# Kernel optimization log

Hardware: AMD Instinct MI355X
Metric: run time of the kernel (lower is better)

Reference implementation:

```python
import jax, jax.numpy as jnp
import numpy as np

N = 100000
E = 3200000
IN_DIM = 512
HID = [64, 32, 16]
OUT_DIM = 40
BN_EPS = 1e-5


def setup_inputs() -> dict:
    key = jax.random.key(0)
    ks = jax.random.split(key, 10)
    x = jax.random.normal(ks[0], (N, IN_DIM), dtype=jnp.float32)
    edge_row = jnp.sort(jax.random.randint(ks[1], (E,), 0, N, dtype=jnp.int32))
    edge_col = jax.random.randint(ks[2], (E,), 0, N, dtype=jnp.int32)
    edge_val = jax.random.uniform(ks[3], (E,), dtype=jnp.float32)

    def xavier(k, fan_in, fan_out):
        limit = np.sqrt(6.0 / (fan_in + fan_out)).astype(np.float32)
        return jax.random.uniform(k, (fan_in, fan_out), dtype=jnp.float32, minval=-limit, maxval=limit)

    W1 = xavier(ks[4], IN_DIM, HID[0])
    W2 = xavier(ks[5], HID[0], HID[1])
    W3 = xavier(ks[6], HID[1], HID[2])
    W4 = xavier(ks[7], HID[2], OUT_DIM)
    return {
        "x": x, "edge_row": edge_row, "edge_col": edge_col, "edge_val": edge_val,
        "W1": W1, "W2": W2, "W3": W3, "W4": W4,
        "g1": jnp.ones((HID[0],), jnp.float32), "b1": jnp.zeros((HID[0],), jnp.float32),
        "g2": jnp.ones((HID[1],), jnp.float32), "b2": jnp.zeros((HID[1],), jnp.float32),
        "g3": jnp.ones((HID[2],), jnp.float32), "b3": jnp.zeros((HID[2],), jnp.float32),
    }


def _gcn_layer(h, W, edge_row, edge_col, edge_val, n_nodes):
    # support = h @ W  (dense GEMM), then SpMM: out[i] = sum_{e: row[e]=i} val[e] * support[col[e]]
    support = h @ W
    msgs = edge_val[:, None] * support[edge_col]  # gather + scale
    return jax.ops.segment_sum(msgs, edge_row, num_segments=n_nodes)


def _bn_elu(h, gamma, beta):
    # BatchNorm1d in training mode: batch statistics over the node dim, biased variance
    mean = jnp.mean(h, axis=0)
    var = jnp.var(h, axis=0)
    h = (h - mean) * jax.lax.rsqrt(var + BN_EPS) * gamma + beta
    return jax.nn.elu(h)


def reference(x, edge_row, edge_col, edge_val, W1, W2, W3, W4, g1, b1, g2, b2, g3, b3):
    n = x.shape[0]
    h = _gcn_layer(x, W1, edge_row, edge_col, edge_val, n)
    h = _bn_elu(h, g1, b1)  # dropout is identity in eval mode
    h = _gcn_layer(h, W2, edge_row, edge_col, edge_val, n)
    h = _bn_elu(h, g2, b2)
    h = _gcn_layer(h, W3, edge_row, edge_col, edge_val, n)
    h = _bn_elu(h, g3, b3)
    h = _gcn_layer(h, W4, edge_row, edge_col, edge_val, n)
    return jax.nn.log_softmax(h, axis=1)
```

## Files before the change

### kernel.cpp

```cpp
#include <hip/hip_runtime.h>
#include <hip/hip_bf16.h>
#include <math.h>

typedef __attribute__((ext_vector_type(8))) short short8;
typedef __attribute__((ext_vector_type(4))) float floatx4;

__global__ void rowptr_k(const int* __restrict__ erow, int* __restrict__ rp, int n, int e) {
    int i = blockIdx.x * blockDim.x + threadIdx.x;
    if (i > n) return;
    int lo = 0, hi = e;
    while (lo < hi) {
        int mid = (lo + hi) >> 1;
        if (erow[mid] < i) lo = mid + 1; else hi = mid;
    }
    rp[i] = lo;
}

__global__ void zero_k(float* __restrict__ p) {
    int i = threadIdx.x;
    if (i < 224) p[i] = 0.f;
}

__device__ __forceinline__ float elu_f(float t) {
    return t > 0.f ? t : expm1f(t);
}

__device__ __forceinline__ unsigned short f2bf(float f) {
    unsigned int u = __float_as_uint(f);
    u = (u + 0x7FFFu + ((u >> 16) & 1u)) >> 16;
    return (unsigned short)u;
}

__device__ __forceinline__ unsigned int f2bf2(float lo, float hi) {
    unsigned int a = __float_as_uint(lo);
    unsigned int b = __float_as_uint(hi);
    a = (a + 0x7FFFu + ((a >> 16) & 1u)) >> 16;
    b = (b + 0x7FFFu + ((b >> 16) & 1u)) & 0xFFFF0000u;
    return a | b;
}

__global__ __launch_bounds__(256) void w1bf_k(const float* __restrict__ W,
                                              unsigned short* __restrict__ Wb) {
    int idx = blockIdx.x * 256 + threadIdx.x;
    int n = idx >> 9, k = idx & 511;
    Wb[idx] = f2bf(W[(long)k * 64 + n]);
}

__global__ __launch_bounds__(256) void gemm1_mfma_k(const float* __restrict__ X,
                                                    const unsigned short* __restrict__ Wb,
                                                    float* __restrict__ out, int nrows) {
    const int lane = threadIdx.x & 63;
    const int wid  = threadIdx.x >> 6;
    const int lrow = lane & 15;
    const int quad = lane >> 4;
    const int m0   = (blockIdx.x * 4 + wid) * 16;
    if (m0 >= nrows) return;

    int arow = m0 + lrow;
    if (arow >= nrows) arow = nrows - 1;
    const float* __restrict__ xrow = X + (long)arow * 512 + quad * 8;
    const unsigned short* __restrict__ brow = Wb + lrow * 512 + quad * 8;

    floatx4 acc[4];
#pragma unroll
    for (int ni = 0; ni < 4; ++ni) acc[ni] = (floatx4){0.f, 0.f, 0.f, 0.f};

    float4 ca0 = *(const float4*)(xrow + 0);
    float4 ca1 = *(const float4*)(xrow + 4);
    short8 cb[4];
#pragma unroll
    for (int ni = 0; ni < 4; ++ni) cb[ni] = *(const short8*)(brow + ni * 8192);

#pragma unroll
    for (int kc = 0; kc < 16; ++kc) {
        float4 na0, na1;
        short8 nb[4];
        if (kc < 15) {
            const float* xp = xrow + (kc + 1) * 32;
            na0 = *(const float4*)(xp + 0);
            na1 = *(const float4*)(xp + 4);
#pragma unroll
            for (int ni = 0; ni < 4; ++ni)
                nb[ni] = *(const short8*)(brow + ni * 8192 + (kc + 1) * 32);
        }
        union { short8 s; unsigned int u[4]; } af;
        af.u[0] = f2bf2(ca0.x, ca0.y);
        af.u[1] = f2bf2(ca0.z, ca0.w);
        af.u[2] = f2bf2(ca1.x, ca1.y);
        af.u[3] = f2bf2(ca1.z, ca1.w);
#pragma unroll
        for (int ni = 0; ni < 4; ++ni)
            acc[ni] = __builtin_amdgcn_mfma_f32_16x16x32_bf16(af.s, cb[ni], acc[ni], 0, 0, 0);
        if (kc < 15) {
            ca0 = na0; ca1 = na1;
#pragma unroll
            for (int ni = 0; ni < 4; ++ni) cb[ni] = nb[ni];
        }
    }

#pragma unroll
    for (int r = 0; r < 4; ++r) {
        int gr = m0 + quad * 4 + r;
        if (gr < nrows) {
#pragma unroll
            for (int ni = 0; ni < 4; ++ni)
                out[(long)gr * 64 + ni * 16 + lrow] = acc[ni][r];
        }
    }
}

template<int K, int NC, bool BN>
__global__ __launch_bounds__(256) void gemm_k(const float* __restrict__ X,
                                              const float* __restrict__ W,
                                              const float* __restrict__ stats,
                                              const float* __restrict__ gamma,
                                              const float* __restrict__ beta,
                                              float* __restrict__ out, int nrows) {
    constexpr int KT = (K < 64) ? K : 64;
    constexpr int S  = KT + 4;
    __shared__ float xs[64 * S];
    __shared__ float ws[KT * NC];
    __shared__ float sc[KT];
    __shared__ float sh[KT];

    const int tid  = threadIdx.x;
    const int c    = tid & 63;
    const int rg   = tid >> 6;
    const int row0 = blockIdx.x * 64;

    if (BN) {
        if (tid < K) {
            float s1 = stats[tid], s2 = stats[K + tid];
            float mean = s1 / (float)nrows;
            float var  = s2 / (float)nrows - mean * mean;
            float rstd = rsqrtf(var + 1e-5f);
            float scl  = gamma[tid] * rstd;
            sc[tid] = scl;
            sh[tid] = beta[tid] - mean * scl;
        }
        __syncthreads();
    }

    float acc[16];
#pragma unroll
    for (int i = 0; i < 16; ++i) acc[i] = 0.f;

    for (int k0 = 0; k0 < K; k0 += KT) {
        for (int idx = tid * 4; idx < 64 * KT; idx += 1024) {
            int r = idx / KT, k = idx - r * KT;
            int gr = row0 + r;
            float4 v = make_float4(0.f, 0.f, 0.f, 0.f);
            if (gr < nrows) v = *(const float4*)&X[(long)gr * K + k0 + k];
            if (BN) {
                v.x = elu_f(v.x * sc[k + 0] + sh[k + 0]);
                v.y = elu_f(v.y * sc[k + 1] + sh[k + 1]);
                v.z = elu_f(v.z * sc[k + 2] + sh[k + 2]);
                v.w = elu_f(v.w * sc[k + 3] + sh[k + 3]);
            }
            *(float4*)&xs[r * S + k] = v;
        }
        for (int idx = tid * 4; idx < KT * NC; idx += 1024) {
            *(float4*)&ws[idx] = *(const float4*)&W[k0 * NC + idx];
        }
        __syncthreads();

        if (c < NC) {
            for (int kk = 0; kk < KT; kk += 4) {
                float w0 = ws[(kk + 0) * NC + c];
                float w1 = ws[(kk + 1) * NC + c];
                float w2 = ws[(kk + 2) * NC + c];
                float w3 = ws[(kk + 3) * NC + c];
#pragma unroll
                for (int i = 0; i < 16; ++i) {
                    const float4 xv = *(const float4*)&xs[(rg * 16 + i) * S + kk];
                    acc[i] += xv.x * w0 + xv.y * w1 + xv.z * w2 + xv.w * w3;
                }
            }
        }
        __syncthreads();
    }

    if (c < NC) {
#pragma unroll
        for (int i = 0; i < 16; ++i) {
            int gr = row0 + rg * 16 + i;
            if (gr < nrows) out[(long)gr * NC + c] = acc[i];
        }
    }
}

template<int F>
__global__ __launch_bounds__(256) void spmm_k(const int* __restrict__ rp,
                                              const int* __restrict__ ecol,
                                              const float* __restrict__ ev,
                                              const float* __restrict__ sup,
                                              float* __restrict__ out, int n) {
    constexpr int NPW = 64 / F;
    const int lane = threadIdx.x & 63;
    const int wid  = (blockIdx.x * blockDim.x + threadIdx.x) >> 6;
    const int sub  = lane / F;
    const int c    = lane - sub * F;
    const int node = wid * NPW + sub;
    if (node >= n) return;
    int s = rp[node], e = rp[node + 1];
    if (NPW == 1) {
        s = __builtin_amdgcn_readfirstlane(s);
        e = __builtin_amdgcn_readfirstlane(e);
    }
    const float* __restrict__ supc = sup + c;
    float a0 = 0.f, a1 = 0.f, a2 = 0.f, a3 = 0.f;
    int i = s;
    for (; i + 8 <= e; i += 8) {
        int   k0 = ecol[i + 0], k1 = ecol[i + 1], k2 = ecol[i + 2], k3 = ecol[i + 3];
        int   k4 = ecol[i + 4], k5 = ecol[i + 5], k6 = ecol[i + 6], k7 = ecol[i + 7];
        float v0 = ev[i + 0], v1 = ev[i + 1], v2 = ev[i + 2], v3 = ev[i + 3];
        float v4 = ev[i + 4], v5 = ev[i + 5], v6 = ev[i + 6], v7 = ev[i + 7];
        float g0 = supc[(long)k0 * F], g1 = supc[(long)k1 * F];
        float g2 = supc[(long)k2 * F], g3 = supc[(long)k3 * F];
        float g4 = supc[(long)k4 * F], g5 = supc[(long)k5 * F];
        float g6 = supc[(long)k6 * F], g7 = supc[(long)k7 * F];
        a0 += v0 * g0; a1 += v1 * g1; a2 += v2 * g2; a3 += v3 * g3;
        a0 += v4 * g4; a1 += v5 * g5; a2 += v6 * g6; a3 += v7 * g7;
    }
    for (; i < e; ++i) a0 += ev[i] * supc[(long)ecol[i] * F];
    out[(long)node * F + c] = (a0 + a1) + (a2 + a3);
}

__global__ __launch_bounds__(256) void spmm4_k(const int* __restrict__ rp,
                                               const int* __restrict__ ecol,
                                               const float* __restrict__ ev,
                                               const float* __restrict__ sup,
                                               float* __restrict__ out, int n) {
    const int lane = threadIdx.x & 63;
    const int node = (blockIdx.x * blockDim.x + threadIdx.x) >> 6;
    const bool valid = (lane < 40) && (node < n);
    float acc = -INFINITY;
    if (node < n) {
        int s = rp[node], e = rp[node + 1];
        s = __builtin_amdgcn_readfirstlane(s);
        e = __builtin_amdgcn_readfirstlane(e);
        if (lane < 40) {
            const float* __restrict__ supc = sup + lane;
            float a0 = 0.f, a1 = 0.f, a2 = 0.f, a3 = 0.f;
            int i = s;
            for (; i + 8 <= e; i += 8) {
                int   k0 = ecol[i + 0], k1 = ecol[i + 1], k2 = ecol[i + 2], k3 = ecol[i + 3];
                int   k4 = ecol[i + 4], k5 = ecol[i + 5], k6 = ecol[i + 6], k7 = ecol[i + 7];
                float v0 = ev[i + 0], v1 = ev[i + 1], v2 = ev[i + 2], v3 = ev[i + 3];
                float v4 = ev[i + 4], v5 = ev[i + 5], v6 = ev[i + 6], v7 = ev[i + 7];
                float g0 = supc[(long)k0 * 40], g1 = supc[(long)k1 * 40];
                float g2 = supc[(long)k2 * 40], g3 = supc[(long)k3 * 40];
                float g4 = supc[(long)k4 * 40], g5 = supc[(long)k5 * 40];
                float g6 = supc[(long)k6 * 40], g7 = supc[(long)k7 * 40];
                a0 += v0 * g0; a1 += v1 * g1; a2 += v2 * g2; a3 += v3 * g3;
                a0 += v4 * g4; a1 += v5 * g5; a2 += v6 * g6; a3 += v7 * g7;
            }
            for (; i < e; ++i) a0 += ev[i] * supc[(long)ecol[i] * 40];
            acc = (a0 + a1) + (a2 + a3);
        }
    }
    float m = acc;
#pragma unroll
    for (int o = 32; o; o >>= 1) m = fmaxf(m, __shfl_xor(m, o, 64));
    float p = valid ? expf(acc - m) : 0.f;
    float ssum = p;
#pragma unroll
    for (int o = 32; o; o >>= 1) ssum += __shfl_xor(ssum, o, 64);
    if (valid) out[(long)node * 40 + lane] = acc - m - logf(ssum);
}

template<int F>
__global__ __launch_bounds__(256) void stats_k(const float* __restrict__ h,
                                               float* __restrict__ stats, int n) {
    __shared__ float sm1[256];
    __shared__ float sm2[256];
    const int tid = threadIdx.x;
    float s1 = 0.f, s2 = 0.f;
    const long total = (long)n * F;
    for (long idx = (long)blockIdx.x * 256 + tid; idx < total; idx += (long)gridDim.x * 256) {
        float v = h[idx];
        s1 += v;
        s2 += v * v;
    }
    sm1[tid] = s1;
    sm2[tid] = s2;
    __syncthreads();
    if (tid < F) {
#pragma unroll
        for (int j = 1; j < 256 / F; ++j) {
            s1 += sm1[tid + j * F];
            s2 += sm2[tid + j * F];
        }
        atomicAdd(&stats[tid], s1);
        atomicAdd(&stats[F + tid], s2);
    }
}

extern "C" void kernel_launch(void* const* d_in, const int* in_sizes, int n_in,
                              void* d_out, int out_size, void* d_ws, size_t ws_size,
                              hipStream_t stream) {
    const float* x    = (const float*)d_in[0];
    const int*   erow = (const int*)d_in[1];
    const int*   ecol = (const int*)d_in[2];
    const float* ev   = (const float*)d_in[3];
    const float* W1   = (const float*)d_in[4];
    const float* W2   = (const float*)d_in[5];
    const float* W3   = (const float*)d_in[6];
    const float* W4   = (const float*)d_in[7];
    const float* g1   = (const float*)d_in[8];
    const float* b1   = (const float*)d_in[9];
    const float* g2   = (const float*)d_in[10];
    const float* b2   = (const float*)d_in[11];
    const float* g3   = (const float*)d_in[12];
    const float* b3   = (const float*)d_in[13];

    const int N = in_sizes[0] / 512;
    const int E = in_sizes[1];

    char* w = (char*)d_ws;
    int* rp = (int*)w;
    size_t off = (((size_t)(N + 1) * 4) + 255) & ~(size_t)255;
    float* stats = (float*)(w + off);
    float* A = stats + 256;
    float* B = A + (size_t)N * 64;
    unsigned short* Wb = (unsigned short*)(B + (size_t)N * 64);
    float* outp = (float*)d_out;

    const int gblocks = (N + 63) / 64;

    rowptr_k<<<(N + 1 + 255) / 256, 256, 0, stream>>>(erow, rp, N, E);
    zero_k<<<1, 256, 0, stream>>>(stats);
    w1bf_k<<<128, 256, 0, stream>>>(W1, Wb);

    {
        int mfrags = (N + 15) / 16;
        gemm1_mfma_k<<<(mfrags + 3) / 4, 256, 0, stream>>>(x, Wb, A, N);
    }
    spmm_k<64><<<(N + 3) / 4, 256, 0, stream>>>(rp, ecol, ev, A, B, N);
    stats_k<64><<<512, 256, 0, stream>>>(B, stats, N);

    gemm_k<64, 32, true><<<gblocks, 256, 0, stream>>>(B, W2, stats, g1, b1, A, N);
    {
        int waves = (N + 1) / 2;
        spmm_k<32><<<(waves + 3) / 4, 256, 0, stream>>>(rp, ecol, ev, A, B, N);
    }
    stats_k<32><<<512, 256, 0, stream>>>(B, stats + 128, N);

    gemm_k<32, 16, true><<<gblocks, 256, 0, stream>>>(B, W3, stats + 128, g2, b2, A, N);
    {
        int waves = (N + 3) / 4;
        spmm_k<16><<<(waves + 3) / 4, 256, 0, stream>>>(rp, ecol, ev, A, B, N);
    }
    stats_k<16><<<512, 256, 0, stream>>>(B, stats + 192, N);

    gemm_k<16, 40, true><<<gblocks, 256, 0, stream>>>(B, W4, stats + 192, g3, b3, A, N);
    spmm4_k<<<(N + 3) / 4, 256, 0, stream>>>(rp, ecol, ev, A, outp, N);
}
```

Before: 789.5 us.

## Store intermediates in bf16, use MFMA for small GEMMs, edge-parallel SpMM

Intermediate feature matrices are now stored as bf16 instead of fp32, which halves gather and stream traffic in the SpMM, stats and GEMM kernels. The small hidden-layer GEMMs move from scalar FMA in shared memory to bf16 MFMA, with BN+ELU fused into the A-operand load. The SpMM kernels now assign one wavefront per node and spread that node's edges across lane groups, each lane loading a vector of bf16 features, then reduce across lanes with shuffles. The cost is bf16 rounding of activations and of the small weights, which lowers accuracy.

```diff
diff --git a/kernel.cpp b/kernel.cpp
--- a/kernel.cpp
+++ b/kernel.cpp
@@ -39,6 +39,9 @@
     return a | b;
 }
 
+__device__ __forceinline__ float bflo(unsigned int d) { return __uint_as_float(d << 16); }
+__device__ __forceinline__ float bfhi(unsigned int d) { return __uint_as_float(d & 0xFFFF0000u); }
+
 __global__ __launch_bounds__(256) void w1bf_k(const float* __restrict__ W,
                                               unsigned short* __restrict__ Wb) {
     int idx = blockIdx.x * 256 + threadIdx.x;
@@ -46,9 +49,30 @@
     Wb[idx] = f2bf(W[(long)k * 64 + n]);
 }
 
+__global__ __launch_bounds__(256) void wsmall_k(const float* __restrict__ W2,
+                                                const float* __restrict__ W3,
+                                                const float* __restrict__ W4,
+                                                unsigned short* __restrict__ Wb2,
+                                                unsigned short* __restrict__ Wb3,
+                                                unsigned short* __restrict__ Wb4) {
+    int idx = blockIdx.x * 256 + threadIdx.x;
+    if (idx < 2048) {
+        int n = idx >> 6, k = idx & 63;
+        Wb2[idx] = f2bf(W2[(long)k * 32 + n]);
+    }
+    if (idx < 512) {
+        int n = idx >> 5, k = idx & 31;
+        Wb3[idx] = f2bf(W3[(long)k * 16 + n]);
+    }
+    if (idx < 1536) {
+        int n = idx >> 5, k = idx & 31;
+        Wb4[idx] = (n < 40 && k < 16) ? f2bf(W4[(long)k * 40 + n]) : (unsigned short)0;
+    }
+}
+
 __global__ __launch_bounds__(256) void gemm1_mfma_k(const float* __restrict__ X,
                                                     const unsigned short* __restrict__ Wb,
-                                                    float* __restrict__ out, int nrows) {
+                                                    unsigned short* __restrict__ out, int nrows) {
     const int lane = threadIdx.x & 63;
     const int wid  = threadIdx.x >> 6;
     const int lrow = lane & 15;
@@ -104,195 +128,211 @@
         if (gr < nrows) {
 #pragma unroll
             for (int ni = 0; ni < 4; ++ni)
-                out[(long)gr * 64 + ni * 16 + lrow] = acc[ni][r];
-        }
-    }
-}
-
-template<int K, int NC, bool BN>
-__global__ __launch_bounds__(256) void gemm_k(const float* __restrict__ X,
-                                              const float* __restrict__ W,
-                                              const float* __restrict__ stats,
-                                              const float* __restrict__ gamma,
-                                              const float* __restrict__ beta,
-                                              float* __restrict__ out, int nrows) {
-    constexpr int KT = (K < 64) ? K : 64;
-    constexpr int S  = KT + 4;
-    __shared__ float xs[64 * S];
-    __shared__ float ws[KT * NC];
-    __shared__ float sc[KT];
-    __shared__ float sh[KT];
-
-    const int tid  = threadIdx.x;
-    const int c    = tid & 63;
-    const int rg   = tid >> 6;
-    const int row0 = blockIdx.x * 64;
-
-    if (BN) {
-        if (tid < K) {
-            float s1 = stats[tid], s2 = stats[K + tid];
-            float mean = s1 / (float)nrows;
-            float var  = s2 / (float)nrows - mean * mean;
-            float rstd = rsqrtf(var + 1e-5f);
-            float scl  = gamma[tid] * rstd;
-            sc[tid] = scl;
-            sh[tid] = beta[tid] - mean * scl;
-        }
-        __syncthreads();
-    }
-
-    float acc[16];
-#pragma unroll
-    for (int i = 0; i < 16; ++i) acc[i] = 0.f;
-
-    for (int k0 = 0; k0 < K; k0 += KT) {
-        for (int idx = tid * 4; idx < 64 * KT; idx += 1024) {
-            int r = idx / KT, k = idx - r * KT;
-            int gr = row0 + r;
-            float4 v = make_float4(0.f, 0.f, 0.f, 0.f);
-            if (gr < nrows) v = *(const float4*)&X[(long)gr * K + k0 + k];
-            if (BN) {
-                v.x = elu_f(v.x * sc[k + 0] + sh[k + 0]);
-                v.y = elu_f(v.y * sc[k + 1] + sh[k + 1]);
-                v.z = elu_f(v.z * sc[k + 2] + sh[k + 2]);
-                v.w = elu_f(v.w * sc[k + 3] + sh[k + 3]);
-            }
-            *(float4*)&xs[r * S + k] = v;
-        }
-        for (int idx = tid * 4; idx < KT * NC; idx += 1024) {
-            *(float4*)&ws[idx] = *(const float4*)&W[k0 * NC + idx];
-        }
-        __syncthreads();
-
-        if (c < NC) {
-            for (int kk = 0; kk < KT; kk += 4) {
-                float w0 = ws[(kk + 0) * NC + c];
-                float w1 = ws[(kk + 1) * NC + c];
-                float w2 = ws[(kk + 2) * NC + c];
-                float w3 = ws[(kk + 3) * NC + c];
-#pragma unroll
-                for (int i = 0; i < 16; ++i) {
-                    const float4 xv = *(const float4*)&xs[(rg * 16 + i) * S + kk];
-                    acc[i] += xv.x * w0 + xv.y * w1 + xv.z * w2 + xv.w * w3;
-                }
-            }
-        }
-        __syncthreads();
-    }
-
-    if (c < NC) {
-#pragma unroll
-        for (int i = 0; i < 16; ++i) {
-            int gr = row0 + rg * 16 + i;
-            if (gr < nrows) out[(long)gr * NC + c] = acc[i];
+                out[(long)gr * 64 + ni * 16 + lrow] = f2bf(acc[ni][r]);
+        }
+    }
+}
+
+template<int K, int KP, int NF, int NSTR>
+__global__ __launch_bounds__(256) void gemmS_k(const unsigned short* __restrict__ H,
+                                               const unsigned short* __restrict__ Wb,
+                                               const float* __restrict__ stats,
+                                               const float* __restrict__ gamma,
+                                               const float* __restrict__ beta,
+                                               unsigned short* __restrict__ out,
+                                               int nrows) {
+    __shared__ __align__(16) float scs[K];
+    __shared__ __align__(16) float shs[K];
+    const int tid = threadIdx.x;
+    if (tid < K) {
+        float s1 = stats[tid], s2 = stats[K + tid];
+        float mean = s1 / (float)nrows;
+        float var  = s2 / (float)nrows - mean * mean;
+        float rstd = rsqrtf(var + 1e-5f);
+        float scl  = gamma[tid] * rstd;
+        scs[tid] = scl;
+        shs[tid] = beta[tid] - mean * scl;
+    }
+    __syncthreads();
+
+    const int lane = tid & 63;
+    const int wid  = tid >> 6;
+    const int lrow = lane & 15;
+    const int quad = lane >> 4;
+    const int m0   = (blockIdx.x * 4 + wid) * 16;
+    if (m0 >= nrows) return;
+
+    int arow = m0 + lrow;
+    if (arow >= nrows) arow = nrows - 1;
+    const unsigned short* __restrict__ hrow = H + (long)arow * K;
+
+    floatx4 acc[NF];
+#pragma unroll
+    for (int ni = 0; ni < NF; ++ni) acc[ni] = (floatx4){0.f, 0.f, 0.f, 0.f};
+
+#pragma unroll
+    for (int kc = 0; kc < KP; kc += 32) {
+        const int k8 = kc + quad * 8;
+        union { short8 s; unsigned int u[4]; } af;
+        if (k8 < K) {
+            uint4 d = *(const uint4*)(hrow + k8);
+            float4 sc0 = *(const float4*)&scs[k8];
+            float4 sc1 = *(const float4*)&scs[k8 + 4];
+            float4 sh0 = *(const float4*)&shs[k8];
+            float4 sh1 = *(const float4*)&shs[k8 + 4];
+            float f0 = elu_f(bflo(d.x) * sc0.x + sh0.x);
+            float f1 = elu_f(bfhi(d.x) * sc0.y + sh0.y);
+            float f2 = elu_f(bflo(d.y) * sc0.z + sh0.z);
+            float f3 = elu_f(bfhi(d.y) * sc0.w + sh0.w);
+            float f4 = elu_f(bflo(d.z) * sc1.x + sh1.x);
+            float f5 = elu_f(bfhi(d.z) * sc1.y + sh1.y);
+            float f6 = elu_f(bflo(d.w) * sc1.z + sh1.z);
+            float f7 = elu_f(bfhi(d.w) * sc1.w + sh1.w);
+            af.u[0] = f2bf2(f0, f1);
+            af.u[1] = f2bf2(f2, f3);
+            af.u[2] = f2bf2(f4, f5);
+            af.u[3] = f2bf2(f6, f7);
+        } else {
+            af.u[0] = af.u[1] = af.u[2] = af.u[3] = 0u;
+        }
+#pragma unroll
+        for (int ni = 0; ni < NF; ++ni) {
+            short8 bf = *(const short8*)&Wb[(ni * 16 + lrow) * KP + k8];
+            acc[ni] = __builtin_amdgcn_mfma_f32_16x16x32_bf16(af.s, bf, acc[ni], 0, 0, 0);
+        }
+    }
+
+#pragma unroll
+    for (int r = 0; r < 4; ++r) {
+        int gr = m0 + quad * 4 + r;
+        if (gr < nrows) {
+#pragma unroll
+            for (int ni = 0; ni < NF; ++ni)
+                out[(long)gr * NSTR + ni * 16 + lrow] = f2bf(acc[ni][r]);
         }
     }
 }
 
 template<int F>
-__global__ __launch_bounds__(256) void spmm_k(const int* __restrict__ rp,
-                                              const int* __restrict__ ecol,
-                                              const float* __restrict__ ev,
-                                              const float* __restrict__ sup,
-                                              float* __restrict__ out, int n) {
-    constexpr int NPW = 64 / F;
-    const int lane = threadIdx.x & 63;
-    const int wid  = (blockIdx.x * blockDim.x + threadIdx.x) >> 6;
-    const int sub  = lane / F;
-    const int c    = lane - sub * F;
-    const int node = wid * NPW + sub;
-    if (node >= n) return;
-    int s = rp[node], e = rp[node + 1];
-    if (NPW == 1) {
-        s = __builtin_amdgcn_readfirstlane(s);
-        e = __builtin_amdgcn_readfirstlane(e);
-    }
-    const float* __restrict__ supc = sup + c;
-    float a0 = 0.f, a1 = 0.f, a2 = 0.f, a3 = 0.f;
-    int i = s;
-    for (; i + 8 <= e; i += 8) {
-        int   k0 = ecol[i + 0], k1 = ecol[i + 1], k2 = ecol[i + 2], k3 = ecol[i + 3];
-        int   k4 = ecol[i + 4], k5 = ecol[i + 5], k6 = ecol[i + 6], k7 = ecol[i + 7];
-        float v0 = ev[i + 0], v1 = ev[i + 1], v2 = ev[i + 2], v3 = ev[i + 3];
-        float v4 = ev[i + 4], v5 = ev[i + 5], v6 = ev[i + 6], v7 = ev[i + 7];
-        float g0 = supc[(long)k0 * F], g1 = supc[(long)k1 * F];
-        float g2 = supc[(long)k2 * F], g3 = supc[(long)k3 * F];
-        float g4 = supc[(long)k4 * F], g5 = supc[(long)k5 * F];
-        float g6 = supc[(long)k6 * F], g7 = supc[(long)k7 * F];
-        a0 += v0 * g0; a1 += v1 * g1; a2 += v2 * g2; a3 += v3 * g3;
-        a0 += v4 * g4; a1 += v5 * g5; a2 += v6 * g6; a3 += v7 * g7;
-    }
-    for (; i < e; ++i) a0 += ev[i] * supc[(long)ecol[i] * F];
-    out[(long)node * F + c] = (a0 + a1) + (a2 + a3);
-}
-
-__global__ __launch_bounds__(256) void spmm4_k(const int* __restrict__ rp,
+__global__ __launch_bounds__(256) void spmmb_k(const int* __restrict__ rp,
                                                const int* __restrict__ ecol,
                                                const float* __restrict__ ev,
-                                               const float* __restrict__ sup,
-                                               float* __restrict__ out, int n) {
+                                               const unsigned short* __restrict__ sup,
+                                               unsigned short* __restrict__ out, int n) {
+    constexpr int GL = F / 4;
+    constexpr int G  = 64 / GL;
     const int lane = threadIdx.x & 63;
     const int node = (blockIdx.x * blockDim.x + threadIdx.x) >> 6;
-    const bool valid = (lane < 40) && (node < n);
-    float acc = -INFINITY;
-    if (node < n) {
-        int s = rp[node], e = rp[node + 1];
-        s = __builtin_amdgcn_readfirstlane(s);
-        e = __builtin_amdgcn_readfirstlane(e);
-        if (lane < 40) {
-            const float* __restrict__ supc = sup + lane;
-            float a0 = 0.f, a1 = 0.f, a2 = 0.f, a3 = 0.f;
-            int i = s;
-            for (; i + 8 <= e; i += 8) {
-                int   k0 = ecol[i + 0], k1 = ecol[i + 1], k2 = ecol[i + 2], k3 = ecol[i + 3];
-                int   k4 = ecol[i + 4], k5 = ecol[i + 5], k6 = ecol[i + 6], k7 = ecol[i + 7];
-                float v0 = ev[i + 0], v1 = ev[i + 1], v2 = ev[i + 2], v3 = ev[i + 3];
-                float v4 = ev[i + 4], v5 = ev[i + 5], v6 = ev[i + 6], v7 = ev[i + 7];
-                float g0 = supc[(long)k0 * 40], g1 = supc[(long)k1 * 40];
-                float g2 = supc[(long)k2 * 40], g3 = supc[(long)k3 * 40];
-                float g4 = supc[(long)k4 * 40], g5 = supc[(long)k5 * 40];
-                float g6 = supc[(long)k6 * 40], g7 = supc[(long)k7 * 40];
-                a0 += v0 * g0; a1 += v1 * g1; a2 += v2 * g2; a3 += v3 * g3;
-                a0 += v4 * g4; a1 += v5 * g5; a2 += v6 * g6; a3 += v7 * g7;
-            }
-            for (; i < e; ++i) a0 += ev[i] * supc[(long)ecol[i] * 40];
-            acc = (a0 + a1) + (a2 + a3);
-        }
-    }
-    float m = acc;
-#pragma unroll
-    for (int o = 32; o; o >>= 1) m = fmaxf(m, __shfl_xor(m, o, 64));
-    float p = valid ? expf(acc - m) : 0.f;
-    float ssum = p;
-#pragma unroll
-    for (int o = 32; o; o >>= 1) ssum += __shfl_xor(ssum, o, 64);
-    if (valid) out[(long)node * 40 + lane] = acc - m - logf(ssum);
+    if (node >= n) return;
+    int s = __builtin_amdgcn_readfirstlane(rp[node]);
+    int e = __builtin_amdgcn_readfirstlane(rp[node + 1]);
+    const int g = lane / GL, p = lane % GL;
+    float a0 = 0.f, a1 = 0.f, a2 = 0.f, a3 = 0.f;
+    for (int i = s; i < e; i += 4 * G) {
+#pragma unroll
+        for (int b = 0; b < 4; ++b) {
+            int idx = i + b * G + g;
+            int cidx = idx < e ? idx : e - 1;
+            int col = ecol[cidx];
+            float v = ev[cidx];
+            if (idx >= e) v = 0.f;
+            uint2 d = *(const uint2*)((const char*)sup + (unsigned long long)col * (F * 2) + p * 8);
+            a0 += v * bflo(d.x);
+            a1 += v * bfhi(d.x);
+            a2 += v * bflo(d.y);
+            a3 += v * bfhi(d.y);
+        }
+    }
+#pragma unroll
+    for (int o = GL; o < 64; o <<= 1) {
+        a0 += __shfl_xor(a0, o, 64);
+        a1 += __shfl_xor(a1, o, 64);
+        a2 += __shfl_xor(a2, o, 64);
+        a3 += __shfl_xor(a3, o, 64);
+    }
+    if (lane < GL) {
+        ushort4 o4;
+        o4.x = f2bf(a0); o4.y = f2bf(a1); o4.z = f2bf(a2); o4.w = f2bf(a3);
+        *(ushort4*)&out[(long)node * F + p * 4] = o4;
+    }
+}
+
+__global__ __launch_bounds__(256) void spmm4b_k(const int* __restrict__ rp,
+                                                const int* __restrict__ ecol,
+                                                const float* __restrict__ ev,
+                                                const unsigned short* __restrict__ sup,
+                                                float* __restrict__ out, int n) {
+    const int lane = threadIdx.x & 63;
+    const int node = (blockIdx.x * blockDim.x + threadIdx.x) >> 6;
+    if (node >= n) return;
+    int s = __builtin_amdgcn_readfirstlane(rp[node]);
+    int e = __builtin_amdgcn_readfirstlane(rp[node + 1]);
+    const int g = lane >> 4, p = lane & 15;
+    float a0 = 0.f, a1 = 0.f, a2 = 0.f, a3 = 0.f;
+    for (int i = s; i < e; i += 16) {
+#pragma unroll
+        for (int b = 0; b < 4; ++b) {
+            int idx = i + b * 4 + g;
+            int cidx = idx < e ? idx : e - 1;
+            int col = ecol[cidx];
+            float v = ev[cidx];
+            if (idx >= e || p >= 12) v = 0.f;
+            uint2 d = *(const uint2*)((const char*)sup + (unsigned long long)col * 96 + p * 8);
+            a0 += v * bflo(d.x);
+            a1 += v * bfhi(d.x);
+            a2 += v * bflo(d.y);
+            a3 += v * bfhi(d.y);
+        }
+    }
+#pragma unroll
+    for (int o = 16; o < 64; o <<= 1) {
+        a0 += __shfl_xor(a0, o, 64);
+        a1 += __shfl_xor(a1, o, 64);
+        a2 += __shfl_xor(a2, o, 64);
+        a3 += __shfl_xor(a3, o, 64);
+    }
+    const bool valid = p < 10;
+    float lm = valid ? fmaxf(fmaxf(a0, a1), fmaxf(a2, a3)) : -INFINITY;
+#pragma unroll
+    for (int o = 1; o < 16; o <<= 1) lm = fmaxf(lm, __shfl_xor(lm, o, 64));
+    float ls = valid ? (expf(a0 - lm) + expf(a1 - lm) + expf(a2 - lm) + expf(a3 - lm)) : 0.f;
+#pragma unroll
+    for (int o = 1; o < 16; o <<= 1) ls += __shfl_xor(ls, o, 64);
+    float lse = lm + logf(ls);
+    if (lane < 10) {
+        float4 o4 = make_float4(a0 - lse, a1 - lse, a2 - lse, a3 - lse);
+        *(float4*)&out[(long)node * 40 + p * 4] = o4;
+    }
 }
 
 template<int F>
-__global__ __launch_bounds__(256) void stats_k(const float* __restrict__ h,
-                                               float* __restrict__ stats, int n) {
-    __shared__ float sm1[256];
-    __shared__ float sm2[256];
+__global__ __launch_bounds__(256) void statsb_k(const unsigned short* __restrict__ h,
+                                                float* __restrict__ stats, int n) {
+    __shared__ float m1[256], m2[256], m3[256], m4[256];
     const int tid = threadIdx.x;
-    float s1 = 0.f, s2 = 0.f;
-    const long total = (long)n * F;
+    const unsigned int* h2 = (const unsigned int*)h;
+    const long total = (long)n * F / 2;
+    float s1 = 0.f, s2 = 0.f, t1 = 0.f, t2 = 0.f;
     for (long idx = (long)blockIdx.x * 256 + tid; idx < total; idx += (long)gridDim.x * 256) {
-        float v = h[idx];
-        s1 += v;
-        s2 += v * v;
-    }
-    sm1[tid] = s1;
-    sm2[tid] = s2;
+        unsigned int d = h2[idx];
+        float lo = bflo(d), hi = bfhi(d);
+        s1 += lo; s2 += lo * lo;
+        t1 += hi; t2 += hi * hi;
+    }
+    m1[tid] = s1; m2[tid] = s2; m3[tid] = t1; m4[tid] = t2;
     __syncthreads();
-    if (tid < F) {
-#pragma unroll
-        for (int j = 1; j < 256 / F; ++j) {
-            s1 += sm1[tid + j * F];
-            s2 += sm2[tid + j * F];
-        }
-        atomicAdd(&stats[tid], s1);
-        atomicAdd(&stats[F + tid], s2);
+    if (tid < F / 2) {
+#pragma unroll 4
+        for (int j = 1; j < 256 / (F / 2); ++j) {
+            s1 += m1[tid + j * (F / 2)];
+            s2 += m2[tid + j * (F / 2)];
+            t1 += m3[tid + j * (F / 2)];
+            t2 += m4[tid + j * (F / 2)];
+        }
+        atomicAdd(&stats[2 * tid], s1);
+        atomicAdd(&stats[2 * tid + 1], t1);
+        atomicAdd(&stats[F + 2 * tid], s2);
+        atomicAdd(&stats[F + 2 * tid + 1], t2);
     }
 }
 
@@ -321,38 +361,34 @@
     int* rp = (int*)w;
     size_t off = (((size_t)(N + 1) * 4) + 255) & ~(size_t)255;
     float* stats = (float*)(w + off);
-    float* A = stats + 256;
-    float* B = A + (size_t)N * 64;
-    unsigned short* Wb = (unsigned short*)(B + (size_t)N * 64);
+    unsigned short* Abf = (unsigned short*)(stats + 256);
+    unsigned short* Bbf = Abf + (size_t)N * 64;
+    unsigned short* Wb1 = Bbf + (size_t)N * 64;
+    unsigned short* Wb2 = Wb1 + 64 * 512;
+    unsigned short* Wb3 = Wb2 + 32 * 64;
+    unsigned short* Wb4 = Wb3 + 16 * 32;
     float* outp = (float*)d_out;
-
-    const int gblocks = (N + 63) / 64;
 
     rowptr_k<<<(N + 1 + 255) / 256, 256, 0, stream>>>(erow, rp, N, E);
     zero_k<<<1, 256, 0, stream>>>(stats);
-    w1bf_k<<<128, 256, 0, stream>>>(W1, Wb);
-
-    {
-        int mfrags = (N + 15) / 16;
-        gemm1_mfma_k<<<(mfrags + 3) / 4, 256, 0, stream>>>(x, Wb, A, N);
-    }
-    spmm_k<64><<<(N + 3) / 4, 256, 0, stream>>>(rp, ecol, ev, A, B, N);
-    stats_k<64><<<512, 256, 0, stream>>>(B, stats, N);
-
-    gemm_k<64, 32, true><<<gblocks, 256, 0, stream>>>(B, W2, stats, g1, b1, A, N);
-    {
-        int waves = (N + 1) / 2;
-        spmm_k<32><<<(waves + 3) / 4, 256, 0, stream>>>(rp, ecol, ev, A, B, N);
-    }
-    stats_k<32><<<512, 256, 0, stream>>>(B, stats + 128, N);
-
-    gemm_k<32, 16, true><<<gblocks, 256, 0, stream>>>(B, W3, stats + 128, g2, b2, A, N);
-    {
-        int waves = (N + 3) / 4;
-        spmm_k<16><<<(waves + 3) / 4, 256, 0, stream>>>(rp, ecol, ev, A, B, N);
-    }
-    stats_k<16><<<512, 256, 0, stream>>>(B, stats + 192, N);
-
-    gemm_k<16, 40, true><<<gblocks, 256, 0, stream>>>(B, W4, stats + 192, g3, b3, A, N);
-    spmm4_k<<<(N + 3) / 4, 256, 0, stream>>>(rp, ecol, ev, A, outp, N);
-}
+    w1bf_k<<<128, 256, 0, stream>>>(W1, Wb1);
+    wsmall_k<<<8, 256, 0, stream>>>(W2, W3, W4, Wb2, Wb3, Wb4);
+
+    const int mblocks = ((N + 15) / 16 + 3) / 4;
+    const int sblocks = (N * 64 + 255) / 256;
+
+    gemm1_mfma_k<<<mblocks, 256, 0, stream>>>(x, Wb1, Abf, N);
+    spmmb_k<64><<<sblocks, 256, 0, stream>>>(rp, ecol, ev, Abf, Bbf, N);
+    statsb_k<64><<<512, 256, 0, stream>>>(Bbf, stats, N);
+
+    gemmS_k<64, 64, 2, 32><<<mblocks, 256, 0, stream>>>(Bbf, Wb2, stats, g1, b1, Abf, N);
+    spmmb_k<32><<<sblocks, 256, 0, stream>>>(rp, ecol, ev, Abf, Bbf, N);
+    statsb_k<32><<<512, 256, 0, stream>>>(Bbf, stats + 128, N);
+
+    gemmS_k<32, 32, 1, 16><<<mblocks, 256, 0, stream>>>(Bbf, Wb3, stats + 128, g2, b2, Abf, N);
+    spmmb_k<16><<<sblocks, 256, 0, stream>>>(rp, ecol, ev, Abf, Bbf, N);
+    statsb_k<16><<<512, 256, 0, stream>>>(Bbf, stats + 192, N);
+
+    gemmS_k<16, 32, 3, 48><<<mblocks, 256, 0, stream>>>(Bbf, Wb4, stats + 192, g3, b3, Abf, N);
+    spmm4b_k<<<sblocks, 256, 0, stream>>>(rp, ecol, ev, Abf, outp, N);
+}
```

Measured after the change: 664.9 us. -15.8%, faster.
